# Kernel optimization log

Hardware: AMD Instinct MI355X
Metric: run time of the kernel (lower is better)

The kernel has to match this reference:

```python
import jax, jax.numpy as jnp
import numpy as np

B, R, NB, T = 32, 96, 5, 2048
FEAT_DIM = 64
SPARSITY = 0.2


def _per_band(X, community, W1, b1, W2, b2):
    # X: [R, T] wavelet coeffs for one (batch, band) slice
    n, t = X.shape
    f32 = X.dtype
    # --- functional connectivity (cosine of centered signals == Pearson corr) ---
    Xc = X - X.mean(axis=1, keepdims=True)
    norm = jnp.linalg.norm(Xc, axis=1, keepdims=True)
    norm = jnp.where(norm == 0, 1.0, norm)
    C = (Xc @ Xc.T) / (norm * norm.T)
    C = jnp.nan_to_num(C, nan=0.0)
    C = C * (1.0 - jnp.eye(n, dtype=f32))  # zero diagonal
    # --- quantile sparsification over strict lower triangle ---
    ti, tj = np.tril_indices(n, -1)
    thr = jnp.quantile(jnp.abs(C[ti, tj]), 1.0 - SPARSITY)
    A = C * (jnp.abs(C) >= thr).astype(f32)  # graph_type == 'weighted'
    # --- node features (5-dim, averaged over regions) ---
    mean_f = X.mean(axis=1)
    std_f = jnp.std(X, axis=1, ddof=1)  # torch.std is unbiased
    energy_f = (X ** 2).sum(axis=1)
    maxamp_f = jnp.abs(X).max(axis=1)
    ps = jnp.abs(jnp.fft.fft(X, axis=1)) ** 2
    ps = ps[:, : t // 2]
    s = ps.sum(axis=1, keepdims=True)
    s = jnp.where(s == 0, 1.0, s)
    p = ps / s
    ent_f = -(p * jnp.log(p + 1e-10)).sum(axis=1)
    node5 = jnp.stack([mean_f, std_f, energy_f, maxamp_f, ent_f], axis=1).mean(axis=0)
    # --- graph properties (6-dim) on binarized adjacency ---
    Bm = (A != 0).astype(f32)
    ne = Bm.sum() / 2.0
    density = ne / (n * (n - 1) / 2.0)
    deg = Bm.sum(axis=1)
    avg_deg = deg.mean()
    A2 = Bm @ Bm
    tri = (A2 * Bm).sum() / 6.0
    poss = (deg * (deg - 1.0)).sum() / 2.0
    clus = jnp.where(poss > 0, tri / jnp.where(poss > 0, poss, 1.0), 0.0)
    # global efficiency: safe reciprocal (zero where A+I == 0; original would emit inf)
    denom = Bm + jnp.eye(n, dtype=f32)
    eff = jnp.where(denom > 0, 1.0 / jnp.where(denom > 0, denom, 1.0), 0.0).sum() / (n * (n - 1))
    # approximate modularity with fixed 2-community assignment (deterministic)
    m2 = 2.0 * ne
    m2_safe = jnp.where(m2 > 0, m2, 1.0)
    same = (community[:, None] == community[None, :]) & (~jnp.eye(n, dtype=bool))
    expected = jnp.outer(deg, deg) / m2_safe
    mod = jnp.where(m2 > 0, (same * (Bm - expected)).sum() / m2_safe, 0.0)
    props = jnp.stack([ne, density, avg_deg, clus, eff, mod])
    feat11 = jnp.concatenate([node5, props])  # [11]
    # --- feature encoder MLP (dropout is identity at inference) ---
    h = jnp.maximum(feat11 @ W1.T + b1, 0.0)
    return A, h @ W2.T + b2


def _forward(wavelet_coeffs, frequency_bands, community, W1, b1, W2, b2):
    b, r, nb, t = wavelet_coeffs.shape
    Xs = wavelet_coeffs.transpose(0, 2, 1, 3).reshape(b * nb, r, t)  # [B*NB, R, T]
    A, F = jax.vmap(_per_band, in_axes=(0, None, None, None, None, None))(
        Xs, community, W1, b1, W2, b2)
    return A.reshape(b, nb, r, r), F.reshape(b, nb, -1)


def setup_inputs() -> dict:
    key = jax.random.key(0)
    k0, k1, k2, k3, k4 = jax.random.split(key, 5)
    wavelet_coeffs = jax.random.normal(k0, (B, R, NB, T), dtype=jnp.float32)
    frequency_bands = jax.random.uniform(k1, (NB, 2), dtype=jnp.float32)
    community = jax.random.randint(k2, (R,), 0, 2)
    W1 = jax.random.normal(k3, (32, 11), dtype=jnp.float32) * 0.3
    b1 = jnp.zeros((32,), jnp.float32)
    W2 = jax.random.normal(k4, (FEAT_DIM, 32), dtype=jnp.float32) * 0.18
    b2 = jnp.zeros((FEAT_DIM,), jnp.float32)
    return {"wavelet_coeffs": wavelet_coeffs, "frequency_bands": frequency_bands,
            "community": community, "W1": W1, "b1": b1, "W2": W2, "b2": b2}


def reference(wavelet_coeffs, frequency_bands, community, W1, b1, W2, b2):
    return _forward(wavelet_coeffs, frequency_bands, community, W1, b1, W2, b2)
```

## Files before the change

kernel.cpp:

```cpp
#include <hip/hip_runtime.h>
#include <hip/hip_bf16.h>
#include <math.h>
#include <float.h>

#ifndef M_PI
#define M_PI 3.14159265358979323846
#endif

#define NBANDS 160
#define RR 96
#define TT 2048
#define NTRIL 4560
#define A_ELEMS ((size_t)NBANDS * RR * RR)
#define NBIN 8192
#define MAXCAND 512
#define BKS 64
#define NST (TT / BKS)
#define GPITCH 72
#define FBLK 384

#define PHI(L) ((L) ^ (((L) >> 5) & 31))

typedef float  f32x4  __attribute__((ext_vector_type(4)));
typedef __bf16 bf16x8 __attribute__((ext_vector_type(8)));
typedef __bf16 bf16x4 __attribute__((ext_vector_type(4)));

__device__ inline void blockReduceSum4(double v0, double v1, double v2, double v3,
                                       double* sred, double out[4]) {
    for (int off = 32; off > 0; off >>= 1) {
        v0 += __shfl_down(v0, off, 64);
        v1 += __shfl_down(v1, off, 64);
        v2 += __shfl_down(v2, off, 64);
        v3 += __shfl_down(v3, off, 64);
    }
    int lane = threadIdx.x & 63, wid = threadIdx.x >> 6;
    int nw = blockDim.x >> 6;
    if (lane == 0) {
        sred[wid * 4 + 0] = v0; sred[wid * 4 + 1] = v1;
        sred[wid * 4 + 2] = v2; sred[wid * 4 + 3] = v3;
    }
    __syncthreads();
    if (threadIdx.x < 4) {
        double r = sred[threadIdx.x];
        for (int w = 1; w < nw; w++) r += sred[w * 4 + threadIdx.x];
        sred[nw * 4 + threadIdx.x] = r;
    }
    __syncthreads();
    out[0] = sred[nw * 4 + 0]; out[1] = sred[nw * 4 + 1];
    out[2] = sred[nw * 4 + 2]; out[3] = sred[nw * 4 + 3];
    __syncthreads();
}

__device__ inline void blockReduceSum2(double v0, double v1,
                                       double* sred, double out[2]) {
    for (int off = 32; off > 0; off >>= 1) {
        v0 += __shfl_down(v0, off, 64);
        v1 += __shfl_down(v1, off, 64);
    }
    int lane = threadIdx.x & 63, wid = threadIdx.x >> 6;
    int nw = blockDim.x >> 6;
    if (lane == 0) { sred[wid * 2 + 0] = v0; sred[wid * 2 + 1] = v1; }
    __syncthreads();
    if (threadIdx.x < 2) {
        double r = sred[threadIdx.x];
        for (int w = 1; w < nw; w++) r += sred[w * 2 + threadIdx.x];
        sred[nw * 2 + threadIdx.x] = r;
    }
    __syncthreads();
    out[0] = sred[nw * 2 + 0]; out[1] = sred[nw * 2 + 1];
    __syncthreads();
}

__device__ inline void blockReduceMax2(double v0, double v1,
                                       double* sred, double out[2]) {
    for (int off = 32; off > 0; off >>= 1) {
        v0 = fmax(v0, __shfl_down(v0, off, 64));
        v1 = fmax(v1, __shfl_down(v1, off, 64));
    }
    int lane = threadIdx.x & 63, wid = threadIdx.x >> 6;
    int nw = blockDim.x >> 6;
    if (lane == 0) { sred[wid * 2 + 0] = v0; sred[wid * 2 + 1] = v1; }
    __syncthreads();
    if (threadIdx.x < 2) {
        double r = sred[threadIdx.x];
        for (int w = 1; w < nw; w++) r = fmax(r, sred[w * 2 + threadIdx.x]);
        sred[nw * 2 + threadIdx.x] = r;
    }
    __syncthreads();
    out[0] = sred[nw * 2 + 0]; out[1] = sred[nw * 2 + 1];
    __syncthreads();
}

__global__ void twiddle_kernel(float* tw) {
    int k = blockIdx.x * blockDim.x + threadIdx.x;
    if (k < 1024) {
        double ang = -2.0 * M_PI * (double)k / 2048.0;
        tw[2 * k]     = (float)cos(ang);
        tw[2 * k + 1] = (float)sin(ang);
    }
}

#define BFLY(r1, r2, WR, WI) do { \
    float _wr = (WR), _wi = (WI); \
    float _tr = _wr * yr[r2] - _wi * yi[r2]; \
    float _ti = _wr * yi[r2] + _wi * yr[r2]; \
    yr[r2] = yr[r1] - _tr; yi[r2] = yi[r1] - _ti; \
    yr[r1] += _tr; yi[r1] += _ti; } while (0)

__global__ __launch_bounds__(256) void rowstat_fft_kernel(
    const float* __restrict__ wc, const float* __restrict__ tw,
    double* __restrict__ rowstats, int goff)
{
    __shared__ float re[TT];
    __shared__ float im[TT];
    __shared__ double sred[32];
    __shared__ float bcast[4];

    int t = threadIdx.x;
    int g0 = (blockIdx.x + goff) * 2;
    int g1 = g0 + 1;

    int band = g0 / RR, r0 = g0 % RR;
    int b = band / 5, nb = band % 5;
    size_t base0 = ((size_t)(b * RR + r0) * 5 + nb) * TT;
    size_t base1 = base0 + (size_t)5 * TT;
    const float2* twv = (const float2*)tw;

    float s0 = 0.f, s1 = 0.f, q0 = 0.f, q1 = 0.f, m0 = 0.f, m1 = 0.f;
#pragma unroll
    for (int c = 0; c < 8; c++) {
        int i = t + c * 256;
        float af = wc[base0 + i];
        float bf = wc[base1 + i];
        int P = PHI(i);
        re[P] = af; im[P] = bf;
        s0 += af; s1 += bf;
        q0 = fmaf(af, af, q0); q1 = fmaf(bf, bf, q1);
        m0 = fmaxf(m0, fabsf(af)); m1 = fmaxf(m1, fabsf(bf));
    }
    __syncthreads();

    double S4[4], M2[2];
    blockReduceSum4((double)s0, (double)s1, (double)q0, (double)q1, sred, S4);
    blockReduceMax2((double)m0, (double)m1, sred, M2);
    double SUM0 = S4[0], SUM1 = S4[1], SQ0 = S4[2], SQ1 = S4[3];
    double MX0 = M2[0], MX1 = M2[1];

    float yr[8], yi[8];

#pragma unroll
    for (int j = 0; j < 8; j++) {
        int p = 8 * t + j;
        int L = (int)(__brev((unsigned)p) >> 21);
        int P = PHI(L);
        yr[j] = re[P]; yi[j] = im[P];
    }

    const float RC = 0.70710678f;
    BFLY(0, 1, 1.0f, 0.0f); BFLY(2, 3, 1.0f, 0.0f);
    BFLY(4, 5, 1.0f, 0.0f); BFLY(6, 7, 1.0f, 0.0f);
    BFLY(0, 2, 1.0f, 0.0f); BFLY(1, 3, 0.0f, -1.0f);
    BFLY(4, 6, 1.0f, 0.0f); BFLY(5, 7, 0.0f, -1.0f);
    BFLY(0, 4, 1.0f, 0.0f); BFLY(1, 5, RC, -RC);
    BFLY(2, 6, 0.0f, -1.0f); BFLY(3, 7, -RC, -RC);

    __syncthreads();
#pragma unroll
    for (int j = 0; j < 8; j++) {
        int P = PHI(8 * t + j);
        re[P] = yr[j]; im[P] = yi[j];
    }
    __syncthreads();
    int oo = t & 7;
    int bb64 = 4 * ((t >> 3) & 7) + (t >> 6);
#pragma unroll
    for (int k = 0; k < 8; k++) {
        int P = PHI(64 * bb64 + 8 * k + oo);
        yr[k] = re[P]; yi[k] = im[P];
    }

    {
        float2 w0 = twv[oo << 7];
        BFLY(0, 1, w0.x, w0.y); BFLY(2, 3, w0.x, w0.y);
        BFLY(4, 5, w0.x, w0.y); BFLY(6, 7, w0.x, w0.y);
        float2 wa = twv[oo << 6];
        float2 wb = twv[(oo + 8) << 6];
        BFLY(0, 2, wa.x, wa.y); BFLY(1, 3, wb.x, wb.y);
        BFLY(4, 6, wa.x, wa.y); BFLY(5, 7, wb.x, wb.y);
        float2 wc0 = twv[oo << 5], wc1 = twv[(oo + 8) << 5];
        float2 wc2 = twv[(oo + 16) << 5], wc3 = twv[(oo + 24) << 5];
        BFLY(0, 4, wc0.x, wc0.y);
        BFLY(1, 5, wc1.x, wc1.y);
        BFLY(2, 6, wc2.x, wc2.y);
        BFLY(3, 7, wc3.x, wc3.y);
    }

    __syncthreads();
#pragma unroll
    for (int k = 0; k < 8; k++) {
        int P = PHI(64 * bb64 + 8 * k + oo);
        re[P] = yr[k]; im[P] = yi[k];
    }
    __syncthreads();
    int O3 = t & 63, Wq = t >> 6;
#pragma unroll
    for (int s = 0; s < 2; s++) {
        int B3 = Wq + 4 * s;
#pragma unroll
        for (int k = 0; k < 4; k++) {
            int P = PHI(256 * B3 + 64 * k + O3);
            yr[4 * s + k] = re[P]; yi[4 * s + k] = im[P];
        }
    }

    {
        float2 w0 = twv[O3 << 4];
        float2 wa = twv[O3 << 3];
        float2 wb = twv[(O3 + 64) << 3];
        BFLY(0, 1, w0.x, w0.y); BFLY(2, 3, w0.x, w0.y);
        BFLY(4, 5, w0.x, w0.y); BFLY(6, 7, w0.x, w0.y);
        BFLY(0, 2, wa.x, wa.y); BFLY(1, 3, wb.x, wb.y);
        BFLY(4, 6, wa.x, wa.y); BFLY(5, 7, wb.x, wb.y);
    }

    __syncthreads();
#pragma unroll
    for (int s = 0; s < 2; s++) {
        int B3 = Wq + 4 * s;
#pragma unroll
        for (int k = 0; k < 4; k++) {
            int P = PHI(256 * B3 + 64 * k + O3);
            re[P] = yr[4 * s + k]; im[P] = yi[4 * s + k];
        }
    }
    __syncthreads();
#pragma unroll
    for (int k = 0; k < 8; k++) {
        int P = PHI(256 * k + t);
        yr[k] = re[P]; yi[k] = im[P];
    }

    {
        float2 w0 = twv[t << 2];
        float2 wa = twv[t << 1];
        float2 wb = twv[(t + 256) << 1];
        BFLY(0, 1, w0.x, w0.y); BFLY(2, 3, w0.x, w0.y);
        BFLY(4, 5, w0.x, w0.y); BFLY(6, 7, w0.x, w0.y);
        BFLY(0, 2, wa.x, wa.y); BFLY(1, 3, wb.x, wb.y);
        BFLY(4, 6, wa.x, wa.y); BFLY(5, 7, wb.x, wb.y);
        float2 wf0 = twv[t], wf1 = twv[t + 256];
        float2 wf2 = twv[t + 512], wf3 = twv[t + 768];
        BFLY(0, 4, wf0.x, wf0.y);
        BFLY(1, 5, wf1.x, wf1.y);
        BFLY(2, 6, wf2.x, wf2.y);
        BFLY(3, 7, wf3.x, wf3.y);
    }

    __syncthreads();
#pragma unroll
    for (int k = 0; k < 8; k++) {
        int P = PHI(256 * k + t);
        re[P] = yr[k]; im[P] = yi[k];
    }
    __syncthreads();

    float psa[8], psb[8];
#pragma unroll
    for (int k = 0; k < 8; k++) {
        int q = (2048 - t - 256 * k) & 2047;
        int P = PHI(q);
        float prr = re[P], pii = im[P];
        float sr = yr[k] + prr, di = yi[k] - pii;
        float si = yi[k] + pii, dr = yr[k] - prr;
        psa[k] = 0.25f * (sr * sr + di * di);
        psb[k] = 0.25f * (si * si + dr * dr);
    }

    float la = 0.f, lb = 0.f;
#pragma unroll
    for (int k = 0; k < 8; k++) { la += psa[k]; lb += psb[k]; }
    double SS[2];
    blockReduceSum2((double)la, (double)lb, sred, SS);
    double SAall = SS[0], SBall = SS[1];
    if (t == 0) {
        bcast[0] = psa[0]; bcast[1] = psa[4];
        bcast[2] = psb[0]; bcast[3] = psb[4];
    }
    __syncthreads();
    double Sa = 0.5 * (SAall + (double)bcast[0] - (double)bcast[1]);
    double Sb = 0.5 * (SBall + (double)bcast[2] - (double)bcast[3]);
    if (Sa == 0.0) Sa = 1.0;
    if (Sb == 0.0) Sb = 1.0;
    float invSa = (float)(1.0 / Sa), invSb = (float)(1.0 / Sb);

    float ea = 0.f, eb = 0.f;
#pragma unroll
    for (int k = 0; k < 8; k++) {
        float pa = psa[k] * invSa;
        float pb = psb[k] * invSb;
        ea += pa * __logf(pa + 1e-10f);
        eb += pb * __logf(pb + 1e-10f);
    }
    double EE[2];
    blockReduceSum2((double)ea, (double)eb, sred, EE);
    double EAall = EE[0], EBall = EE[1];

    if (t == 0) {
        float pa0 = psa[0] * invSa, pa4 = psa[4] * invSa;
        float pb0 = psb[0] * invSb, pb4 = psb[4] * invSb;
        double TA = 0.5 * (EAall + (double)(pa0 * __logf(pa0 + 1e-10f))
                                 - (double)(pa4 * __logf(pa4 + 1e-10f)));
        double TB = 0.5 * (EBall + (double)(pb0 * __logf(pb0 + 1e-10f))
                                 - (double)(pb4 * __logf(pb4 + 1e-10f)));
        double mean0 = SUM0 / (double)TT;
        double mean1 = SUM1 / (double)TT;
        double nsq0 = SQ0 - (double)TT * mean0 * mean0; if (nsq0 < 0) nsq0 = 0;
        double nsq1 = SQ1 - (double)TT * mean1 * mean1; if (nsq1 < 0) nsq1 = 0;
        double* w0 = rowstats + (size_t)g0 * 6;
        double* w1 = rowstats + (size_t)g1 * 6;
        double n0 = sqrt(nsq0), n1 = sqrt(nsq1);
        w0[0] = mean0; w0[1] = (n0 == 0.0 ? 1.0 : n0); w0[2] = sqrt(nsq0 / 2047.0);
        w0[3] = SQ0;   w0[4] = MX0;                    w0[5] = -TA;
        w1[0] = mean1; w1[1] = (n1 == 0.0 ? 1.0 : n1); w1[2] = sqrt(nsq1 / 2047.0);
        w1[3] = SQ1;   w1[4] = MX1;                    w1[5] = -TB;
    }
}

#define CVW(BUF, v, row, c4) do { \
    __bf16 _h0 = (__bf16)v.x, _h1 = (__bf16)v.y, _h2 = (__bf16)v.z, _h3 = (__bf16)v.w; \
    __bf16 _l0 = (__bf16)(v.x - (float)_h0), _l1 = (__bf16)(v.y - (float)_h1); \
    __bf16 _l2 = (__bf16)(v.z - (float)_h2), _l3 = (__bf16)(v.w - (float)_h3); \
    *(bf16x4*)&sh_hi[BUF][row][(c4) * 4] = (bf16x4){_h0, _h1, _h2, _h3}; \
    *(bf16x4*)&sh_lo[BUF][row][(c4) * 4] = (bf16x4){_l0, _l1, _l2, _l3}; } while (0)

__global__ __launch_bounds__(FBLK) void fused_gram_finalize_kernel(
    const float* __restrict__ wc, const double* __restrict__ rowstats,
    const int* __restrict__ community,
    const float* __restrict__ W1, const float* __restrict__ b1,
    const float* __restrict__ W2, const float* __restrict__ b2,
    float* __restrict__ A_out, float* __restrict__ F_out)
{
    __shared__ __attribute__((aligned(16))) __bf16 sh_hi[2][RR][GPITCH];
    __shared__ __attribute__((aligned(16))) __bf16 sh_lo[2][RR][GPITCH];
    __shared__ float Cs[RR][RR];
    __shared__ int hist[NBIN];
    __shared__ int chunkv[256];
    __shared__ int pchunk[256];
    __shared__ int gpre_s[64];
    __shared__ float cand[MAXCAND];
    __shared__ int ctrl[8];
    __shared__ float selv[2];
    __shared__ double mean_s[RR], inv_s[RR];
    __shared__ int comm_s[RR];
    __shared__ unsigned long long msk[RR][2];
    __shared__ int deg[RR];
    __shared__ double sred[32];
    __shared__ double feat[11];
    __shared__ double hmlp[32];
    __shared__ double thr_s;

    int band = blockIdx.x, t = threadIdx.x;
    int b = band / 5, nb = band % 5;
    size_t bandbase = ((size_t)b * RR * 5 + nb) * TT;
    const double* rsb = rowstats + (size_t)band * RR * 6;

    if (t < RR) {
        mean_s[t] = rsb[t * 6 + 0];
        inv_s[t]  = 1.0 / rsb[t * 6 + 1];
        comm_s[t] = community[t];
    }
    for (int i = t; i < NBIN; i += FBLK) hist[i] = 0;
    if (t == 0) ctrl[3] = 0;

    int wave = t >> 6, lane = t & 63;
    int m16 = lane & 15, quad = lane >> 4;
    int arow = wave * 16 + m16;

    int row0 = t >> 4,           c40 = t & 15;
    int row1 = (t + 384) >> 4,   c41 = (t + 384) & 15;
    int row2 = (t + 768) >> 4,   c42 = (t + 768) & 15;
    int row3 = (t + 1152) >> 4,  c43 = (t + 1152) & 15;
    const float* p0 = wc + bandbase + (size_t)row0 * (5 * TT) + c40 * 4;
    const float* p1 = wc + bandbase + (size_t)row1 * (5 * TT) + c41 * 4;
    const float* p2 = wc + bandbase + (size_t)row2 * (5 * TT) + c42 * 4;
    const float* p3 = wc + bandbase + (size_t)row3 * (5 * TT) + c43 * 4;

    f32x4 acc[6];
#pragma unroll
    for (int ct = 0; ct < 6; ct++) acc[ct] = (f32x4){0.f, 0.f, 0.f, 0.f};

    {
        float4 v0 = *(const float4*)(p0);
        float4 v1 = *(const float4*)(p1);
        float4 v2 = *(const float4*)(p2);
        float4 v3 = *(const float4*)(p3);
        CVW(0, v0, row0, c40); CVW(0, v1, row1, c41);
        CVW(0, v2, row2, c42); CVW(0, v3, row3, c43);
    }
    __syncthreads();

    for (int st = 0; st < NST; st++) {
        int cur = st & 1;
        float4 q0, q1, q2, q3;
        bool more = (st + 1 < NST);
        if (more) {
            int k0 = (st + 1) * BKS;
            q0 = *(const float4*)(p0 + k0);
            q1 = *(const float4*)(p1 + k0);
            q2 = *(const float4*)(p2 + k0);
            q3 = *(const float4*)(p3 + k0);
        }
#pragma unroll
        for (int ks = 0; ks < BKS / 32; ks++) {
            int ko = ks * 32 + quad * 8;
            bf16x8 ah = *(const bf16x8*)&sh_hi[cur][arow][ko];
            bf16x8 al = *(const bf16x8*)&sh_lo[cur][arow][ko];
#pragma unroll
            for (int ct = 0; ct < 6; ct++) {
                int brow = ct * 16 + m16;
                bf16x8 bh = *(const bf16x8*)&sh_hi[cur][brow][ko];
                bf16x8 bl = *(const bf16x8*)&sh_lo[cur][brow][ko];
                acc[ct] = __builtin_amdgcn_mfma_f32_16x16x32_bf16(ah, bh, acc[ct], 0, 0, 0);
                acc[ct] = __builtin_amdgcn_mfma_f32_16x16x32_bf16(ah, bl, acc[ct], 0, 0, 0);
                acc[ct] = __builtin_amdgcn_mfma_f32_16x16x32_bf16(al, bh, acc[ct], 0, 0, 0);
            }
        }
        if (more) {
            int nxt = cur ^ 1;
            CVW(nxt, q0, row0, c40); CVW(nxt, q1, row1, c41);
            CVW(nxt, q2, row2, c42); CVW(nxt, q3, row3, c43);
        }
        __syncthreads();
    }

#pragma unroll
    for (int ct = 0; ct < 6; ct++) {
#pragma unroll
        for (int r = 0; r < 4; r++) {
            int grow = wave * 16 + quad * 4 + r;
            int gcol = ct * 16 + m16;
            double cd = ((double)acc[ct][r]
                         - (double)TT * mean_s[grow] * mean_s[gcol])
                        * (inv_s[grow] * inv_s[gcol]);
            if (grow == gcol) cd = 0.0;
            float cf = (float)cd;
            Cs[grow][gcol] = cf;
            if (gcol < grow) {
                float val = fabsf(cf);
                int bin = (int)(val * (float)NBIN);
                bin = bin > (NBIN - 1) ? (NBIN - 1) : bin;
                atomicAdd(&hist[bin], 1);
            }
        }
    }
    __syncthreads();

    if (t < 256) {
        int cs = 0;
#pragma unroll
        for (int i = 0; i < NBIN / 256; i++) cs += hist[t * (NBIN / 256) + i];
        chunkv[t] = cs;
    }
    __syncthreads();
    if (t < 64) {
        int s4 = chunkv[4 * t] + chunkv[4 * t + 1] + chunkv[4 * t + 2] + chunkv[4 * t + 3];
        int inc = s4;
        for (int d = 1; d < 64; d <<= 1) {
            int u = __shfl_up(inc, d, 64);
            if (t >= d) inc += u;
        }
        gpre_s[t] = inc - s4;
    }
    __syncthreads();
    if (t < 256) {
        int base = gpre_s[t >> 2];
        for (int j = (t & ~3); j < t; j++) base += chunkv[j];
        pchunk[t] = base;
    }
    __syncthreads();
    if (t < 256) {
        int lo = pchunk[t], hi2 = lo + chunkv[t];
        if (lo <= 3647 && 3647 < hi2) ctrl[4] = t;
        if (lo <= 3648 && 3648 < hi2) ctrl[5] = t;
    }
    __syncthreads();
    {
        int c0 = ctrl[4], c1 = ctrl[5];
        if (t < 32) {
            int binb = c0 * 32;
            int pre = pchunk[c0];
            for (int j = 0; j < t; j++) pre += hist[binb + j];
            int cnt = hist[binb + t];
            if (pre <= 3647 && 3647 < pre + cnt) { ctrl[0] = binb + t; ctrl[2] = pre; }
        } else if (t < 64) {
            int tt2 = t - 32;
            int binb = c1 * 32;
            int pre = pchunk[c1];
            for (int j = 0; j < tt2; j++) pre += hist[binb + j];
            int cnt = hist[binb + tt2];
            if (pre <= 3648 && 3648 < pre + cnt) ctrl[1] = binb + tt2;
        }
    }
    __syncthreads();

    int B0 = ctrl[0], B1 = ctrl[1];
    for (int idx = t; idx < RR * RR; idx += FBLK) {
        int i = idx / RR, j = idx % RR;
        if (j < i) {
            float val = fabsf(Cs[i][j]);
            int bin = (int)(val * (float)NBIN);
            bin = bin > (NBIN - 1) ? (NBIN - 1) : bin;
            if (bin >= B0 && bin <= B1) {
                int k = atomicAdd(&ctrl[3], 1);
                if (k < MAXCAND) cand[k] = val;
            }
        }
    }
    __syncthreads();

    {
        int n = ctrl[3]; if (n > MAXCAND) n = MAXCAND;
        int r0l = 3647 - ctrl[2];
        int r1l = 3648 - ctrl[2];
        for (int i = t; i < n; i += FBLK) {
            float v = cand[i];
            int rank = 0;
            for (int j = 0; j < n; j++) {
                float u = cand[j];
                rank += (u < v || (u == v && j < i)) ? 1 : 0;
            }
            if (rank == r0l) selv[0] = v;
            if (rank == r1l) selv[1] = v;
        }
    }
    __syncthreads();
    if (t == 0) {
        double v0 = (double)selv[0], v1 = (double)selv[1];
        thr_s = v0 + 0.2 * (v1 - v0);
    }
    __syncthreads();
    double thr = thr_s;

    float* Ab = A_out + (size_t)band * (RR * RR);
    for (int idx = t; idx < RR * RR; idx += FBLK) {
        float cf = Cs[idx / RR][idx % RR];
        bool keep = ((double)fabsf(cf) >= thr);
        Ab[idx] = keep ? cf : 0.f;
    }

    for (int i = wave; i < RR; i += 6) {
        float vlo = Cs[i][lane];
        bool klo = ((double)fabsf(vlo) >= thr) && (vlo != 0.f);
        unsigned long long blo = __ballot(klo);
        float vhi = Cs[i][64 + (lane & 31)];
        bool khi = (lane < 32) && ((double)fabsf(vhi) >= thr) && (vhi != 0.f);
        unsigned long long bhi = __ballot(khi) & 0xffffffffull;
        if (lane == 0) {
            msk[i][0] = blo; msk[i][1] = bhi;
            deg[i] = __popcll(blo) + __popcll(bhi);
        }
    }
    __syncthreads();

    double triord = 0, ein = 0, expin = 0;
    for (int idx = t; idx < RR * RR; idx += FBLK) {
        int i = idx / RR, j = idx % RR;
        unsigned long long mi0 = msk[i][0], mi1 = msk[i][1];
        bool bij = (((j < 64) ? (mi0 >> j) : (mi1 >> (j - 64))) & 1ull) != 0;
        if (bij)
            triord += (double)(__popcll(mi0 & msk[j][0]) +
                               __popcll(mi1 & msk[j][1]));
        if (i != j && comm_s[i] == comm_s[j]) {
            ein += bij ? 1.0 : 0.0;
            expin += (double)deg[i] * (double)deg[j];
        }
    }
    double dv = (t < RR) ? (double)deg[t] : 0.0;
    double R1v[4], R2v[4], R3v[2];
    blockReduceSum4(triord, ein, expin, dv, sred, R1v);
    blockReduceSum4((t < RR) ? dv * (dv - 1.0) : 0.0,
                    (t < RR) ? rsb[t * 6 + 0] : 0.0,
                    (t < RR) ? rsb[t * 6 + 2] : 0.0,
                    (t < RR) ? rsb[t * 6 + 3] : 0.0, sred, R2v);
    blockReduceSum2((t < RR) ? rsb[t * 6 + 4] : 0.0,
                    (t < RR) ? rsb[t * 6 + 5] : 0.0, sred, R3v);
    double TRI = R1v[0], EIN = R1v[1], EXPIN = R1v[2], DEGS = R1v[3];
    double POSS2 = R2v[0], N0 = R2v[1], N1 = R2v[2], N2 = R2v[3];
    double N3 = R3v[0], N4 = R3v[1];

    if (t == 0) {
        double ne = 0.5 * DEGS;
        feat[0] = N0 / (double)RR;
        feat[1] = N1 / (double)RR;
        feat[2] = N2 / (double)RR;
        feat[3] = N3 / (double)RR;
        feat[4] = N4 / (double)RR;
        feat[5] = ne;
        feat[6] = ne / (double)NTRIL;
        feat[7] = DEGS / (double)RR;
        double tri = TRI / 6.0, poss = POSS2 * 0.5;
        feat[8] = (poss > 0.0) ? tri / poss : 0.0;
        feat[9] = ((double)RR + DEGS) / ((double)RR * (double)(RR - 1));
        double m2 = DEGS;
        feat[10] = (m2 > 0.0) ? (EIN - EXPIN / m2) / m2 : 0.0;
    }
    __syncthreads();

    if (t < 32) {
        double a = (double)b1[t];
        for (int k = 0; k < 11; k++) a += (double)W1[t * 11 + k] * feat[k];
        hmlp[t] = (a > 0.0) ? a : 0.0;
    }
    __syncthreads();
    if (t < 64) {
        double a = (double)b2[t];
        for (int j = 0; j < 32; j++) a += (double)W2[t * 32 + j] * hmlp[j];
        F_out[(size_t)band * 64 + t] = (float)a;
    }
}

extern "C" void kernel_launch(void* const* d_in, const int* in_sizes, int n_in,
                              void* d_out, int out_size, void* d_ws, size_t ws_size,
                              hipStream_t stream) {
    const float* wc        = (const float*)d_in[0];
    const int*   community = (const int*)d_in[2];
    const float* W1        = (const float*)d_in[3];
    const float* b1        = (const float*)d_in[4];
    const float* W2        = (const float*)d_in[5];
    const float* b2        = (const float*)d_in[6];

    float* A_out = (float*)d_out;
    float* F_out = A_out + A_ELEMS;

    char* ws = (char*)d_ws;
    float*  tw       = (float*)ws;
    double* rowstats = (double*)(ws + 8192);

    const int HGRID = NBANDS * RR / 4;
    hipLaunchKernelGGL(twiddle_kernel, dim3(4), dim3(256), 0, stream, tw);
    hipLaunchKernelGGL(rowstat_fft_kernel, dim3(HGRID), dim3(256), 0, stream,
                       wc, tw, rowstats, 0);
    hipLaunchKernelGGL(rowstat_fft_kernel, dim3(HGRID), dim3(256), 0, stream,
                       wc, tw, rowstats, HGRID);
    hipLaunchKernelGGL(fused_gram_finalize_kernel, dim3(NBANDS), dim3(FBLK), 0, stream,
                       wc, rowstats, community, W1, b1, W2, b2, A_out, F_out);
}
```

Measured before the change: 316.0 us.

## Retile Gram MFMA loop to 2x3 per-wave blocks and merge FFT launches

Each of the six waves in the Gram kernel now computes a 2x3 block of 16x16 output tiles instead of a 1x6 strip. A fragments are reused across three column tiles and B fragments across two row tiles, which cuts LDS fragment reads per MFMA. The LDS pitch changes from 72 to 76 to avoid bank conflicts, so fragments are now loaded as two 8-byte halves instead of one 16-byte load. The two half-grid rowstat FFT launches are merged into a single launch, removing one launch overhead.

```diff
diff --git a/kernel.cpp b/kernel.cpp
--- a/kernel.cpp
+++ b/kernel.cpp
@@ -16,7 +16,7 @@
 #define MAXCAND 512
 #define BKS 64
 #define NST (TT / BKS)
-#define GPITCH 72
+#define GPITCH 76
 #define FBLK 384
 
 #define PHI(L) ((L) ^ (((L) >> 5) & 31))
@@ -109,7 +109,7 @@
 
 __global__ __launch_bounds__(256) void rowstat_fft_kernel(
     const float* __restrict__ wc, const float* __restrict__ tw,
-    double* __restrict__ rowstats, int goff)
+    double* __restrict__ rowstats)
 {
     __shared__ float re[TT];
     __shared__ float im[TT];
@@ -117,7 +117,7 @@
     __shared__ float bcast[4];
 
     int t = threadIdx.x;
-    int g0 = (blockIdx.x + goff) * 2;
+    int g0 = blockIdx.x * 2;
     int g1 = g0 + 1;
 
     int band = g0 / RR, r0 = g0 % RR;
@@ -332,6 +332,11 @@
     __bf16 _l2 = (__bf16)(v.z - (float)_h2), _l3 = (__bf16)(v.w - (float)_h3); \
     *(bf16x4*)&sh_hi[BUF][row][(c4) * 4] = (bf16x4){_h0, _h1, _h2, _h3}; \
     *(bf16x4*)&sh_lo[BUF][row][(c4) * 4] = (bf16x4){_l0, _l1, _l2, _l3}; } while (0)
+
+#define LDFRAG(dst, arr, BUF, row, ko) do { \
+    bf16x4 _f0 = *(const bf16x4*)&arr[BUF][row][ko]; \
+    bf16x4 _f1 = *(const bf16x4*)&arr[BUF][row][(ko) + 4]; \
+    dst = (bf16x8){_f0[0], _f0[1], _f0[2], _f0[3], _f1[0], _f1[1], _f1[2], _f1[3]}; } while (0)
 
 __global__ __launch_bounds__(FBLK) void fused_gram_finalize_kernel(
     const float* __restrict__ wc, const double* __restrict__ rowstats,
@@ -374,7 +379,8 @@
 
     int wave = t >> 6, lane = t & 63;
     int m16 = lane & 15, quad = lane >> 4;
-    int arow = wave * 16 + m16;
+    int wr = wave >> 1;
+    int wcx = wave & 1;
 
     int row0 = t >> 4,           c40 = t & 15;
     int row1 = (t + 384) >> 4,   c41 = (t + 384) & 15;
@@ -385,9 +391,11 @@
     const float* p2 = wc + bandbase + (size_t)row2 * (5 * TT) + c42 * 4;
     const float* p3 = wc + bandbase + (size_t)row3 * (5 * TT) + c43 * 4;
 
-    f32x4 acc[6];
-#pragma unroll
-    for (int ct = 0; ct < 6; ct++) acc[ct] = (f32x4){0.f, 0.f, 0.f, 0.f};
+    f32x4 acc[2][3];
+#pragma unroll
+    for (int rs = 0; rs < 2; rs++)
+#pragma unroll
+        for (int cs = 0; cs < 3; cs++) acc[rs][cs] = (f32x4){0.f, 0.f, 0.f, 0.f};
 
     {
         float4 v0 = *(const float4*)(p0);
@@ -413,16 +421,25 @@
 #pragma unroll
         for (int ks = 0; ks < BKS / 32; ks++) {
             int ko = ks * 32 + quad * 8;
-            bf16x8 ah = *(const bf16x8*)&sh_hi[cur][arow][ko];
-            bf16x8 al = *(const bf16x8*)&sh_lo[cur][arow][ko];
-#pragma unroll
-            for (int ct = 0; ct < 6; ct++) {
-                int brow = ct * 16 + m16;
-                bf16x8 bh = *(const bf16x8*)&sh_hi[cur][brow][ko];
-                bf16x8 bl = *(const bf16x8*)&sh_lo[cur][brow][ko];
-                acc[ct] = __builtin_amdgcn_mfma_f32_16x16x32_bf16(ah, bh, acc[ct], 0, 0, 0);
-                acc[ct] = __builtin_amdgcn_mfma_f32_16x16x32_bf16(ah, bl, acc[ct], 0, 0, 0);
-                acc[ct] = __builtin_amdgcn_mfma_f32_16x16x32_bf16(al, bh, acc[ct], 0, 0, 0);
+            bf16x8 ah[2], al[2];
+#pragma unroll
+            for (int rs = 0; rs < 2; rs++) {
+                int ar = (wr * 2 + rs) * 16 + m16;
+                LDFRAG(ah[rs], sh_hi, cur, ar, ko);
+                LDFRAG(al[rs], sh_lo, cur, ar, ko);
+            }
+#pragma unroll
+            for (int cs = 0; cs < 3; cs++) {
+                int br = (wcx * 3 + cs) * 16 + m16;
+                bf16x8 bh, bl;
+                LDFRAG(bh, sh_hi, cur, br, ko);
+                LDFRAG(bl, sh_lo, cur, br, ko);
+#pragma unroll
+                for (int rs = 0; rs < 2; rs++) {
+                    acc[rs][cs] = __builtin_amdgcn_mfma_f32_16x16x32_bf16(ah[rs], bh, acc[rs][cs], 0, 0, 0);
+                    acc[rs][cs] = __builtin_amdgcn_mfma_f32_16x16x32_bf16(ah[rs], bl, acc[rs][cs], 0, 0, 0);
+                    acc[rs][cs] = __builtin_amdgcn_mfma_f32_16x16x32_bf16(al[rs], bh, acc[rs][cs], 0, 0, 0);
+                }
             }
         }
         if (more) {
@@ -434,22 +451,25 @@
     }
 
 #pragma unroll
-    for (int ct = 0; ct < 6; ct++) {
-#pragma unroll
-        for (int r = 0; r < 4; r++) {
-            int grow = wave * 16 + quad * 4 + r;
-            int gcol = ct * 16 + m16;
-            double cd = ((double)acc[ct][r]
-                         - (double)TT * mean_s[grow] * mean_s[gcol])
-                        * (inv_s[grow] * inv_s[gcol]);
-            if (grow == gcol) cd = 0.0;
-            float cf = (float)cd;
-            Cs[grow][gcol] = cf;
-            if (gcol < grow) {
-                float val = fabsf(cf);
-                int bin = (int)(val * (float)NBIN);
-                bin = bin > (NBIN - 1) ? (NBIN - 1) : bin;
-                atomicAdd(&hist[bin], 1);
+    for (int rs = 0; rs < 2; rs++) {
+#pragma unroll
+        for (int cs = 0; cs < 3; cs++) {
+#pragma unroll
+            for (int r = 0; r < 4; r++) {
+                int grow = (wr * 2 + rs) * 16 + quad * 4 + r;
+                int gcol = (wcx * 3 + cs) * 16 + m16;
+                double cd = ((double)acc[rs][cs][r]
+                             - (double)TT * mean_s[grow] * mean_s[gcol])
+                            * (inv_s[grow] * inv_s[gcol]);
+                if (grow == gcol) cd = 0.0;
+                float cf = (float)cd;
+                Cs[grow][gcol] = cf;
+                if (gcol < grow) {
+                    float val = fabsf(cf);
+                    int bin = (int)(val * (float)NBIN);
+                    bin = bin > (NBIN - 1) ? (NBIN - 1) : bin;
+                    atomicAdd(&hist[bin], 1);
+                }
             }
         }
     }
@@ -636,12 +656,9 @@
     float*  tw       = (float*)ws;
     double* rowstats = (double*)(ws + 8192);
 
-    const int HGRID = NBANDS * RR / 4;
     hipLaunchKernelGGL(twiddle_kernel, dim3(4), dim3(256), 0, stream, tw);
-    hipLaunchKernelGGL(rowstat_fft_kernel, dim3(HGRID), dim3(256), 0, stream,
-                       wc, tw, rowstats, 0);
-    hipLaunchKernelGGL(rowstat_fft_kernel, dim3(HGRID), dim3(256), 0, stream,
-                       wc, tw, rowstats, HGRID);
+    hipLaunchKernelGGL(rowstat_fft_kernel, dim3(NBANDS * RR / 2), dim3(256), 0, stream,
+                       wc, tw, rowstats);
     hipLaunchKernelGGL(fused_gram_finalize_kernel, dim3(NBANDS), dim3(FBLK), 0, stream,
                        wc, rowstats, community, W1, b1, W2, b2, A_out, F_out);
 }
```

After: 294.7 us. 1.07x faster.
